# Kernel optimization log

Hardware: AMD Instinct MI355X
Metric: run time of the kernel (lower is better)

The kernel has to match this reference:

```python
import jax, jax.numpy as jnp
import numpy as np

B, S, D, H, DFF = 2, 2048, 1024, 16, 4096
DK = D // H
EPS = 1e-5


def layer_norm(x, gamma, beta, eps=EPS):
    mu = jnp.mean(x, axis=-1, keepdims=True)
    var = jnp.mean(jnp.square(x - mu), axis=-1, keepdims=True)
    return (x - mu) * jax.lax.rsqrt(var + eps) * gamma + beta


def setup_inputs() -> dict:
    key = jax.random.key(0)
    ks = jax.random.split(key, 12)
    s_d = 1.0 / np.sqrt(D)
    s_f = 1.0 / np.sqrt(DFF)
    return {
        "x": jax.random.normal(ks[0], (B, S, D), jnp.float32),
        # per-head QKV projections stacked: [H, D, DK]
        "Wq": jax.random.normal(ks[1], (H, D, DK), jnp.float32) * s_d,
        "bq": jnp.zeros((H, DK), jnp.float32),
        "Wk": jax.random.normal(ks[2], (H, D, DK), jnp.float32) * s_d,
        "bk": jnp.zeros((H, DK), jnp.float32),
        "Wv": jax.random.normal(ks[3], (H, D, DK), jnp.float32) * s_d,
        "bv": jnp.zeros((H, DK), jnp.float32),
        "Wo": jax.random.normal(ks[4], (D, D), jnp.float32) * s_d,
        "bo": jnp.zeros((D,), jnp.float32),
        "W1": jax.random.normal(ks[5], (D, DFF), jnp.float32) * s_d,
        "b1": jnp.zeros((DFF,), jnp.float32),
        "W2": jax.random.normal(ks[6], (DFF, D), jnp.float32) * s_f,
        "b2": jnp.zeros((D,), jnp.float32),
        "ln1_g": jnp.ones((D,), jnp.float32),
        "ln1_b": jnp.zeros((D,), jnp.float32),
        "ln2_g": jnp.ones((D,), jnp.float32),
        "ln2_b": jnp.zeros((D,), jnp.float32),
    }


def reference(x, Wq, bq, Wk, bk, Wv, bv, Wo, bo, W1, b1, W2, b2,
              ln1_g, ln1_b, ln2_g, ln2_b):
    # --- residual 1: pre-norm multi-head self-attention (mask unused, dropout=eval) ---
    h = layer_norm(x, ln1_g, ln1_b)                      # [B,S,D]
    q = jnp.einsum('bsd,hdk->bhsk', h, Wq) + bq[:, None, :]
    k = jnp.einsum('bsd,hdk->bhsk', h, Wk) + bk[:, None, :]
    v = jnp.einsum('bsd,hdk->bhsk', h, Wv) + bv[:, None, :]
    scores = jnp.einsum('bhsk,bhtk->bhst', q, k) / np.sqrt(DK)  # [B,H,S,S]
    w = jax.nn.softmax(scores, axis=-1)
    ctx = jnp.einsum('bhst,bhtk->bhsk', w, v)            # [B,H,S,DK]
    # concat heads along feature dim -> [B,S,D]
    ctx = jnp.transpose(ctx, (0, 2, 1, 3)).reshape(B, S, D)
    attn_out = ctx @ Wo + bo
    x = x + attn_out
    # --- residual 2: pre-norm feed-forward ---
    h2 = layer_norm(x, ln2_g, ln2_b)
    ff = jax.nn.relu(h2 @ W1 + b1) @ W2 + b2
    return x + ff
```

## Files before the change

### kernel.cpp

```cpp
#include <hip/hip_runtime.h>

#define B_   2
#define S_   2048
#define D_   1024
#define H_   16
#define DK_  64
#define DFF_ 4096
#define NT_  (B_*S_)
#define QS_  3072

using u16 = unsigned short;
typedef __attribute__((ext_vector_type(8))) short bf16x8;
typedef __attribute__((ext_vector_type(4))) float f32x4;
typedef __attribute__((ext_vector_type(4))) u16  u16x4;

__device__ __forceinline__ float bf2f(u16 h) {
  union { unsigned u; float f; } c; c.u = ((unsigned)h) << 16; return c.f;
}
__device__ __forceinline__ u16 f2bf(float f) {
  union { float f; unsigned u; } c; c.f = f;
  unsigned u = c.u;
  return (u16)((u + 0x7fffu + ((u >> 16) & 1u)) >> 16);
}
__device__ __forceinline__ u16 f2bf_up(float f) {
  union { float f; unsigned u; } c; c.f = f;
  return (u16)((c.u + 0x8000u) >> 16);
}

__device__ __forceinline__ void load_lds16(const void* g, void* l) {
  __builtin_amdgcn_global_load_lds(
      (const __attribute__((address_space(1))) unsigned int*)g,
      (__attribute__((address_space(3))) unsigned int*)l, 16, 0, 0);
}

__device__ __forceinline__ void store_out(u16* p, float v)   { *p = f2bf(v); }
__device__ __forceinline__ void store_out(float* p, float v) { *p = v; }

__global__ __launch_bounds__(256) void ln_kernel(
    const float* __restrict__ x, const float* __restrict__ g,
    const float* __restrict__ bt, u16* __restrict__ o)
{
  const int row = blockIdx.x, t = threadIdx.x;
  const float4 xv = *(const float4*)(x + (size_t)row * D_ + t * 4);
  float f[4] = {xv.x, xv.y, xv.z, xv.w};
  float sum = f[0] + f[1] + f[2] + f[3];
  float sq  = f[0]*f[0] + f[1]*f[1] + f[2]*f[2] + f[3]*f[3];
#pragma unroll
  for (int d = 32; d >= 1; d >>= 1) {
    sum += __shfl_down(sum, d);
    sq  += __shfl_down(sq, d);
  }
  __shared__ float red[8];
  const int lane = t & 63, wid = t >> 6;
  if (lane == 0) { red[wid] = sum; red[wid + 4] = sq; }
  __syncthreads();
  sum = red[0] + red[1] + red[2] + red[3];
  sq  = red[4] + red[5] + red[6] + red[7];
  const float mu   = sum * (1.0f / D_);
  const float var  = sq * (1.0f / D_) - mu * mu;
  const float rstd = rsqrtf(var + 1e-5f);
  const float4 gv = *(const float4*)(g  + t * 4);
  const float4 bv = *(const float4*)(bt + t * 4);
  u16x4 ov;
  ov[0] = f2bf((f[0] - mu) * rstd * gv.x + bv.x);
  ov[1] = f2bf((f[1] - mu) * rstd * gv.y + bv.y);
  ov[2] = f2bf((f[2] - mu) * rstd * gv.z + bv.z);
  ov[3] = f2bf((f[3] - mu) * rstd * gv.w + bv.w);
  *(u16x4*)(o + (size_t)row * D_ + t * 4) = ov;
}

__global__ __launch_bounds__(256) void transpose_h(
    const float* __restrict__ in, u16* __restrict__ out, int R, int C)
{
  __shared__ float tile[32][33];
  const int z = blockIdx.z;
  const float* ip = in  + (size_t)z * R * C;
  u16*         op = out + (size_t)z * R * C;
  const int c0 = blockIdx.x * 32, r0 = blockIdx.y * 32;
  const int tx = threadIdx.x & 31, ty = threadIdx.x >> 5;
#pragma unroll
  for (int i = 0; i < 32; i += 8)
    tile[ty + i][tx] = ip[(size_t)(r0 + ty + i) * C + c0 + tx];
  __syncthreads();
#pragma unroll
  for (int i = 0; i < 32; i += 8)
    op[(size_t)(c0 + ty + i) * R + r0 + tx] = f2bf(tile[tx][ty + i]);
}

__global__ __launch_bounds__(256) void transpose_qkv(
    const float* __restrict__ Wq, const float* __restrict__ Wk,
    const float* __restrict__ Wv, u16* __restrict__ out)
{
  __shared__ float tile[32][33];
  const int z = blockIdx.z;
  const int which = z >> 4, h = z & 15;
  const float* ip = (which == 0 ? Wq : which == 1 ? Wk : Wv) + (size_t)h * 1024 * 64;
  u16* op = out + ((size_t)which * 1024 + h * 64) * 1024;
  const float sc = (which == 0) ? 0.125f : 1.0f;
  const int c0 = blockIdx.x * 32, r0 = blockIdx.y * 32;
  const int tx = threadIdx.x & 31, ty = threadIdx.x >> 5;
#pragma unroll
  for (int i = 0; i < 32; i += 8)
    tile[ty + i][tx] = ip[(size_t)(r0 + ty + i) * 64 + c0 + tx];
  __syncthreads();
#pragma unroll
  for (int i = 0; i < 32; i += 8)
    op[(size_t)(c0 + ty + i) * 1024 + r0 + tx] = f2bf(tile[tx][ty + i] * sc);
}

__global__ __launch_bounds__(256) void transpose_v(
    const u16* __restrict__ qkv, u16* __restrict__ vt)
{
  __shared__ u16 tile[32][33];
  const int z = blockIdx.z;
  const int b = z >> 4, h = z & 15;
  const u16* ip = qkv + (size_t)(b * S_) * QS_ + 2048 + h * DK_;
  u16* op = vt + (size_t)z * DK_ * S_;
  const int t0 = blockIdx.x * 32, d0 = blockIdx.y * 32;
  const int tx = threadIdx.x & 31, ty = threadIdx.x >> 5;
#pragma unroll
  for (int i = 0; i < 32; i += 8)
    tile[ty + i][tx] = ip[(size_t)(t0 + ty + i) * QS_ + d0 + tx];
  __syncthreads();
#pragma unroll
  for (int i = 0; i < 32; i += 8)
    op[(size_t)(d0 + ty + i) * S_ + t0 + tx] = tile[tx][ty + i];
}

template <typename OT>
__global__ __launch_bounds__(256) void gemm_bt(
    const u16* __restrict__ A, const u16* __restrict__ Bt,
    const float* __restrict__ bias, const float* __restrict__ biasB,
    const float* __restrict__ biasC, const float* __restrict__ res,
    OT* __restrict__ C, int M, int N, int K, int do_relu)
{
  __shared__ u16 lA[2][128 * 32];
  __shared__ u16 lB[2][128 * 32];
  const int tid = threadIdx.x, lane = tid & 63, wid = tid >> 6;
  const int wr = wid >> 1, wc = wid & 1;

  const int nbx = gridDim.x;
  int bid = blockIdx.y * nbx + blockIdx.x;
  const int cpx = (nbx * gridDim.y) >> 3;
  bid = (bid & 7) * cpx + (bid >> 3);
  const int row0 = (bid / nbx) * 128, col0 = (bid % nbx) * 128;

  f32x4 acc[4][4] = {};

  const int cc0 = tid, cc1 = tid + 256;
  const int r0 = cc0 >> 2, s0 = cc0 & 3;
  const int r1 = cc1 >> 2, s1 = cc1 & 3;
  const int ko0 = (s0 ^ ((r0 >> 1) & 3)) * 8;
  const int ko1 = (s1 ^ ((r1 >> 1) & 3)) * 8;

#define GST128(bf, k0)                                                        \
  {                                                                           \
    load_lds16(A  + (size_t)(row0 + r0) * K + (k0) + ko0, &lA[bf][cc0 * 8]);  \
    load_lds16(A  + (size_t)(row0 + r1) * K + (k0) + ko1, &lA[bf][cc1 * 8]);  \
    load_lds16(Bt + (size_t)(col0 + r0) * K + (k0) + ko0, &lB[bf][cc0 * 8]);  \
    load_lds16(Bt + (size_t)(col0 + r1) * K + (k0) + ko1, &lB[bf][cc1 * 8]);  \
  }

  const int nk = K >> 5;
  GST128(0, 0);
  int cur = 0;
  for (int t = 0; t < nk; ++t) {
    __syncthreads();
    if (t + 1 < nk) GST128(cur ^ 1, (t + 1) * 32);
    bf16x8 af[4], bfr[4];
#pragma unroll
    for (int m = 0; m < 4; ++m) {
      const int row = wr * 64 + m * 16 + (lane & 15);
      af[m] = *(const bf16x8*)&lA[cur][row * 32 + (((lane >> 4) ^ ((row >> 1) & 3)) * 8)];
    }
#pragma unroll
    for (int n = 0; n < 4; ++n) {
      const int row = wc * 64 + n * 16 + (lane & 15);
      bfr[n] = *(const bf16x8*)&lB[cur][row * 32 + (((lane >> 4) ^ ((row >> 1) & 3)) * 8)];
    }
#pragma unroll
    for (int m = 0; m < 4; ++m)
#pragma unroll
      for (int n = 0; n < 4; ++n)
        acc[m][n] = __builtin_amdgcn_mfma_f32_16x16x32_bf16(af[m], bfr[n], acc[m][n], 0, 0, 0);
    cur ^= 1;
  }
#undef GST128

#pragma unroll
  for (int m = 0; m < 4; ++m)
#pragma unroll
    for (int n = 0; n < 4; ++n) {
      const int rbase = row0 + wr*64 + m*16 + ((lane >> 4) << 2);
      const int c     = col0 + wc*64 + n*16 + (lane & 15);
      float bv = 0.f;
      if (biasC)      bv = c < 1024 ? bias[c] * 0.125f
                         : (c < 2048 ? biasB[c - 1024] : biasC[c - 2048]);
      else if (bias)  bv = bias[c];
#pragma unroll
      for (int r = 0; r < 4; ++r) {
        const int rr = rbase + r;
        float vv = acc[m][n][r] + bv;
        if (res) vv += res[(size_t)rr * N + c];
        if (do_relu) vv = vv > 0.f ? vv : 0.f;
        store_out(&C[(size_t)rr * N + c], vv);
      }
    }
}

template <typename OT, int KK>
__global__ __launch_bounds__(512, 1) void gemm256(
    const u16* __restrict__ A, const u16* __restrict__ Bt,
    const float* __restrict__ bias, OT* __restrict__ C,
    int M, int N, int do_relu)
{
  constexpr int NK = KK / 32;
  __shared__ u16 lA[4][256 * 32];
  __shared__ u16 lB[4][256 * 32];
  const int tid = threadIdx.x, lane = tid & 63, wid = tid >> 6;
  const int wr = wid >> 2, wc = wid & 3;

  const int nbx = gridDim.x;
  int bid = blockIdx.y * nbx + blockIdx.x;
  const int cpx = (nbx * gridDim.y) >> 3;
  bid = (bid & 7) * cpx + (bid >> 3);
  const int row0 = (bid / nbx) * 256, col0 = (bid % nbx) * 256;

  const int c0 = tid,       sr0 = c0 >> 2, q0 = ((c0 & 3) ^ (((sr0 >> 3) & 1) << 1)) * 8;
  const int c1 = tid + 512, sr1 = c1 >> 2, q1 = ((c1 & 3) ^ (((sr1 >> 3) & 1) << 1)) * 8;
  const u16* As0 = A  + (size_t)(row0 + sr0) * KK + q0;
  const u16* As1 = A  + (size_t)(row0 + sr1) * KK + q1;
  const u16* Bs0 = Bt + (size_t)(col0 + sr0) * KK + q0;
  const u16* Bs1 = Bt + (size_t)(col0 + sr1) * KK + q1;

  f32x4 acc[8][4] = {};
  const int lrow = lane & 15, kcol = (lane >> 4) * 8;

#pragma unroll
  for (int t = 0; t < 3; ++t) {
    load_lds16(As0 + t * 32, &lA[t][c0 * 8]);
    load_lds16(Bs0 + t * 32, &lB[t][c0 * 8]);
    load_lds16(As1 + t * 32, &lA[t][c1 * 8]);
    load_lds16(Bs1 + t * 32, &lB[t][c1 * 8]);
  }
  asm volatile("s_waitcnt vmcnt(8)" ::: "memory");
  __builtin_amdgcn_sched_barrier(0);
  __builtin_amdgcn_s_barrier();

#pragma unroll 4
  for (int j = 0; j < NK; ++j) {
    const int b = j & 3;
    const u16* la = lA[b];
    const u16* lb = lB[b];
    bf16x8 af[4], bfr[4];

#pragma unroll
    for (int m = 0; m < 4; ++m) {
      const int row = wr * 128 + m * 16 + lrow;
      af[m] = *(const bf16x8*)&la[row * 32 + (kcol ^ (((row >> 3) & 1) << 4))];
    }
#pragma unroll
    for (int n = 0; n < 4; ++n) {
      const int row = wc * 64 + n * 16 + lrow;
      bfr[n] = *(const bf16x8*)&lb[row * 32 + (kcol ^ (((row >> 3) & 1) << 4))];
    }
    if (j + 3 < NK) {
      const int bb = (j + 3) & 3;
      load_lds16(As0 + (j + 3) * 32, &lA[bb][c0 * 8]);
      load_lds16(Bs0 + (j + 3) * 32, &lB[bb][c0 * 8]);
    }
    __builtin_amdgcn_s_setprio(1);
#pragma unroll
    for (int m = 0; m < 4; ++m)
#pragma unroll
      for (int n = 0; n < 4; ++n)
        acc[m][n] = __builtin_amdgcn_mfma_f32_16x16x32_bf16(af[m], bfr[n], acc[m][n], 0, 0, 0);
    __builtin_amdgcn_s_setprio(0);
    __builtin_amdgcn_sched_barrier(0);
    __builtin_amdgcn_s_barrier();

#pragma unroll
    for (int m = 0; m < 4; ++m) {
      const int row = wr * 128 + (m + 4) * 16 + lrow;
      af[m] = *(const bf16x8*)&la[row * 32 + (kcol ^ (((row >> 3) & 1) << 4))];
    }
    if (j + 3 < NK) {
      const int bb = (j + 3) & 3;
      load_lds16(As1 + (j + 3) * 32, &lA[bb][c1 * 8]);
      load_lds16(Bs1 + (j + 3) * 32, &lB[bb][c1 * 8]);
    }
    __builtin_amdgcn_s_setprio(1);
#pragma unroll
    for (int m = 0; m < 4; ++m)
#pragma unroll
      for (int n = 0; n < 4; ++n)
        acc[m + 4][n] = __builtin_amdgcn_mfma_f32_16x16x32_bf16(af[m], bfr[n], acc[m + 4][n], 0, 0, 0);
    __builtin_amdgcn_s_setprio(0);
    if (j + 3 < NK)      { asm volatile("s_waitcnt vmcnt(8)" ::: "memory"); }
    else if (j + 2 < NK) { asm volatile("s_waitcnt vmcnt(4)" ::: "memory"); }
    else if (j + 1 < NK) { asm volatile("s_waitcnt vmcnt(0)" ::: "memory"); }
    __builtin_amdgcn_sched_barrier(0);
    __builtin_amdgcn_s_barrier();
  }

#pragma unroll
  for (int m = 0; m < 8; ++m)
#pragma unroll
    for (int n = 0; n < 4; ++n) {
      const int rbase = row0 + wr*128 + m*16 + ((lane >> 4) << 2);
      const int c     = col0 + wc*64 + n*16 + (lane & 15);
      const float bv  = bias ? bias[c] : 0.f;
#pragma unroll
      for (int r = 0; r < 4; ++r) {
        float vv = acc[m][n][r] + bv;
        if (do_relu) vv = vv > 0.f ? vv : 0.f;
        store_out(&C[(size_t)(rbase + r) * N + c], vv);
      }
    }
}

template <typename OT>
__global__ __launch_bounds__(256) void gemm_bt64(
    const u16* __restrict__ A, const u16* __restrict__ Bt,
    const float* __restrict__ bias, const float* __restrict__ res,
    OT* __restrict__ C, int M, int N, int K, int do_relu)
{
  __shared__ u16 lA[2][128 * 32];
  __shared__ u16 lB[2][64 * 32];
  const int tid = threadIdx.x, lane = tid & 63, wid = tid >> 6;

  const int nbx = gridDim.x;
  int bid = blockIdx.y * nbx + blockIdx.x;
  const int cpx = (nbx * gridDim.y) >> 3;
  bid = (bid & 7) * cpx + (bid >> 3);
  const int row0 = (bid / nbx) * 128, col0 = (bid % nbx) * 64;

  f32x4 acc[2][4] = {};

  const int cc0 = tid, cc1 = tid + 256;
  const int r0 = cc0 >> 2, s0 = cc0 & 3;
  const int r1 = cc1 >> 2, s1 = cc1 & 3;
  const int ko0 = (s0 ^ ((r0 >> 1) & 3)) * 8;
  const int ko1 = (s1 ^ ((r1 >> 1) & 3)) * 8;

#define GST64(bf, k0)                                                         \
  {                                                                           \
    load_lds16(A  + (size_t)(row0 + r0) * K + (k0) + ko0, &lA[bf][cc0 * 8]);  \
    load_lds16(A  + (size_t)(row0 + r1) * K + (k0) + ko1, &lA[bf][cc1 * 8]);  \
    load_lds16(Bt + (size_t)(col0 + r0) * K + (k0) + ko0, &lB[bf][cc0 * 8]);  \
  }

  const int nk = K >> 5;
  GST64(0, 0);
  int cur = 0;
  for (int t = 0; t < nk; ++t) {
    __syncthreads();
    if (t + 1 < nk) GST64(cur ^ 1, (t + 1) * 32);
    bf16x8 af[2], bfr[4];
#pragma unroll
    for (int m = 0; m < 2; ++m) {
      const int row = wid * 32 + m * 16 + (lane & 15);
      af[m] = *(const bf16x8*)&lA[cur][row * 32 + (((lane >> 4) ^ ((row >> 1) & 3)) * 8)];
    }
#pragma unroll
    for (int n = 0; n < 4; ++n) {
      const int row = n * 16 + (lane & 15);
      bfr[n] = *(const bf16x8*)&lB[cur][row * 32 + (((lane >> 4) ^ ((row >> 1) & 3)) * 8)];
    }
#pragma unroll
    for (int m = 0; m < 2; ++m)
#pragma unroll
      for (int n = 0; n < 4; ++n)
        acc[m][n] = __builtin_amdgcn_mfma_f32_16x16x32_bf16(af[m], bfr[n], acc[m][n], 0, 0, 0);
    cur ^= 1;
  }
#undef GST64

#pragma unroll
  for (int m = 0; m < 2; ++m)
#pragma unroll
    for (int n = 0; n < 4; ++n) {
      const int rbase = row0 + wid*32 + m*16 + ((lane >> 4) << 2);
      const int c     = col0 + n*16 + (lane & 15);
      const float bv  = bias ? bias[c] : 0.f;
#pragma unroll
      for (int r = 0; r < 4; ++r) {
        const int rr = rbase + r;
        float vv = acc[m][n][r] + bv;
        if (res) vv += res[(size_t)rr * N + c];
        if (do_relu) vv = vv > 0.f ? vv : 0.f;
        store_out(&C[(size_t)rr * N + c], vv);
      }
    }
}

__global__ __launch_bounds__(256) void gemm_bt64_pk(
    const u16* __restrict__ A, const u16* __restrict__ Bt,
    float* __restrict__ P, int M, int N, int K, int KS)
{
  __shared__ u16 lA[2][128 * 32];
  __shared__ u16 lB[2][64 * 32];
  const int tid = threadIdx.x, lane = tid & 63, wid = tid >> 6;

  const int nbx = gridDim.x;
  int bid = blockIdx.y * nbx + blockIdx.x;
  const int cpx = (nbx * gridDim.y) >> 3;
  bid = (bid & 7) * cpx + (bid >> 3);
  const int row0 = (bid / nbx) * 128, col0 = (bid % nbx) * 64;
  const int kb = blockIdx.z * KS;

  f32x4 acc[2][4] = {};

  const int cc0 = tid, cc1 = tid + 256;
  const int r0 = cc0 >> 2, s0 = cc0 & 3;
  const int r1 = cc1 >> 2, s1 = cc1 & 3;
  const int ko0 = (s0 ^ ((r0 >> 1) & 3)) * 8;
  const int ko1 = (s1 ^ ((r1 >> 1) & 3)) * 8;

#define GSTPK(bf, k0)                                                              \
  {                                                                                \
    load_lds16(A  + (size_t)(row0 + r0) * K + kb + (k0) + ko0, &lA[bf][cc0 * 8]);  \
    load_lds16(A  + (size_t)(row0 + r1) * K + kb + (k0) + ko1, &lA[bf][cc1 * 8]);  \
    load_lds16(Bt + (size_t)(col0 + r0) * K + kb + (k0) + ko0, &lB[bf][cc0 * 8]);  \
  }

  const int nk = KS >> 5;
  GSTPK(0, 0);
  int cur = 0;
  for (int t = 0; t < nk; ++t) {
    __syncthreads();
    if (t + 1 < nk) GSTPK(cur ^ 1, (t + 1) * 32);
    bf16x8 af[2], bfr[4];
#pragma unroll
    for (int m = 0; m < 2; ++m) {
      const int row = wid * 32 + m * 16 + (lane & 15);
      af[m] = *(const bf16x8*)&lA[cur][row * 32 + (((lane >> 4) ^ ((row >> 1) & 3)) * 8)];
    }
#pragma unroll
    for (int n = 0; n < 4; ++n) {
      const int row = n * 16 + (lane & 15);
      bfr[n] = *(const bf16x8*)&lB[cur][row * 32 + (((lane >> 4) ^ ((row >> 1) & 3)) * 8)];
    }
#pragma unroll
    for (int m = 0; m < 2; ++m)
#pragma unroll
      for (int n = 0; n < 4; ++n)
        acc[m][n] = __builtin_amdgcn_mfma_f32_16x16x32_bf16(af[m], bfr[n], acc[m][n], 0, 0, 0);
    cur ^= 1;
  }
#undef GSTPK

  float* Pz = P + (size_t)blockIdx.z * M * N;
#pragma unroll
  for (int m = 0; m < 2; ++m)
#pragma unroll
    for (int n = 0; n < 4; ++n) {
      const int rbase = row0 + wid*32 + m*16 + ((lane >> 4) << 2);
      const int c     = col0 + n*16 + (lane & 15);
#pragma unroll
      for (int r = 0; r < 4; ++r)
        Pz[(size_t)(rbase + r) * N + c] = acc[m][n][r];
    }
}

__global__ __launch_bounds__(256) void ffr_reduce(
    const float* __restrict__ p0, const float* __restrict__ p1,
    const float* __restrict__ x1, const float* __restrict__ b2,
    float* __restrict__ out)
{
  const size_t i = (size_t)blockIdx.x * 256 + threadIdx.x;
  const float4 a  = ((const float4*)p0)[i];
  const float4 b  = ((const float4*)p1)[i];
  const float4 r  = ((const float4*)x1)[i];
  const float4 bb = ((const float4*)b2)[i & 255];
  float4 o;
  o.x = a.x + b.x + r.x + bb.x;
  o.y = a.y + b.y + r.y + bb.y;
  o.z = a.z + b.z + r.z + bb.z;
  o.w = a.w + b.w + r.w + bb.w;
  ((float4*)out)[i] = o;
}

__global__ __launch_bounds__(512) void attn_kernel(
    const u16* __restrict__ QKV, const u16* __restrict__ Vt, u16* __restrict__ O)
{
  __shared__ u16 lK[2][64 * 64];
  __shared__ u16 lV[2][64 * 64];
  __shared__ u16 lP[128 * 64];

  const int tid = threadIdx.x, lane = tid & 63, wid = tid >> 6;
  const int qt = ((blockIdx.x & 7) << 1) | (blockIdx.x >> 3);
  const int h = blockIdx.y, b = blockIdx.z;

  const u16* Qp = QKV + (size_t)(b * S_ + qt * 128) * QS_ + h * DK_;
  const u16* Kb = QKV + (size_t)(b * S_) * QS_ + 1024 + h * DK_;
  const u16* Vb = Vt  + (size_t)(b * H_ + h) * DK_ * S_;

  bf16x8 qf[2];
  {
    const int qr = wid * 16 + (lane & 15);
    qf[0] = *(const bf16x8*)(Qp + (size_t)qr * QS_ + (lane >> 4) * 8);
    qf[1] = *(const bf16x8*)(Qp + (size_t)qr * QS_ + 32 + (lane >> 4) * 8);
  }

  const bf16x8 vone = {16256,16256,16256,16256,16256,16256,16256,16256};

#define STAGE_KV(bf, kt)                                                      \
  {                                                                           \
    const u16* Kp = Kb + (size_t)(kt) * 64 * QS_;                             \
    const u16* Vp = Vb + (size_t)(kt) * 64;                                   \
    const int c = tid, r = c >> 3, sub = c & 7;                               \
    load_lds16(Kp + (size_t)r * QS_ + ((sub ^ (r & 7)) * 8), &lK[bf][c * 8]); \
    load_lds16(Vp + (size_t)r * S_  + ((sub ^ (r & 7)) * 8), &lV[bf][c * 8]); \
  }

  float m_run = -1e30f;
  f32x4 l_acc = {};
  f32x4 o_acc[4] = {};

  STAGE_KV(0, 0);
  int cur = 0;

  for (int kt = 0; kt < S_ / 64; ++kt) {
    __syncthreads();
    if (kt + 1 < S_ / 64) STAGE_KV(cur ^ 1, kt + 1);

    f32x4 s[4];
    __builtin_amdgcn_s_setprio(1);
#pragma unroll
    for (int kf = 0; kf < 4; ++kf) {
      const int row = kf * 16 + (lane & 15);
      const int i0 = (row * 64 + (lane >> 4) * 8)      ^ ((row & 7) << 3);
      const int i1 = (row * 64 + 32 + (lane >> 4) * 8) ^ ((row & 7) << 3);
      bf16x8 k0 = *(const bf16x8*)&lK[cur][i0];
      bf16x8 k1 = *(const bf16x8*)&lK[cur][i1];
      f32x4 sc = {};
      sc = __builtin_amdgcn_mfma_f32_16x16x32_bf16(k0, qf[0], sc, 0, 0, 0);
      sc = __builtin_amdgcn_mfma_f32_16x16x32_bf16(k1, qf[1], sc, 0, 0, 0);
      s[kf] = sc;
    }
    __builtin_amdgcn_s_setprio(0);

    float t0 = fmaxf(fmaxf(s[0][0], s[0][1]), fmaxf(s[0][2], s[0][3]));
    float t1 = fmaxf(fmaxf(s[1][0], s[1][1]), fmaxf(s[1][2], s[1][3]));
    float t2 = fmaxf(fmaxf(s[2][0], s[2][1]), fmaxf(s[2][2], s[2][3]));
    float t3 = fmaxf(fmaxf(s[3][0], s[3][1]), fmaxf(s[3][2], s[3][3]));
    float pmax = fmaxf(fmaxf(t0, t1), fmaxf(t2, t3));
    pmax = fmaxf(pmax, __shfl_xor(pmax, 16));
    pmax = fmaxf(pmax, __shfl_xor(pmax, 32));

    const bool grow = pmax > m_run + 8.0f;
    const float mnew = grow ? pmax : m_run;
    if (__any(grow)) {
      const float scale = __expf(m_run - mnew);
#pragma unroll
      for (int r = 0; r < 4; ++r) {
        const float sr = __shfl(scale, (lane >> 4) * 4 + r);
        l_acc[r] *= sr;
#pragma unroll
        for (int nf = 0; nf < 4; ++nf) o_acc[nf][r] *= sr;
      }
    }
    m_run = mnew;

    const int prow = wid * 16 + (lane & 15);
#pragma unroll
    for (int kf = 0; kf < 4; ++kf) {
      u16x4 pk;
#pragma unroll
      for (int r = 0; r < 4; ++r) pk[r] = f2bf_up(__expf(s[kf][r] - m_run));
      const int idx = (prow * 64 + kf * 16 + (lane >> 4) * 4) ^ ((prow & 7) << 3);
      *(u16x4*)&lP[idx] = pk;
    }
    asm volatile("s_waitcnt lgkmcnt(0)" ::: "memory");
    __builtin_amdgcn_sched_barrier(0);

    bf16x8 pa0 = *(const bf16x8*)&lP[(prow * 64 + (lane >> 4) * 8)      ^ ((prow & 7) << 3)];
    bf16x8 pa1 = *(const bf16x8*)&lP[(prow * 64 + 32 + (lane >> 4) * 8) ^ ((prow & 7) << 3)];
    __builtin_amdgcn_s_setprio(1);
    l_acc = __builtin_amdgcn_mfma_f32_16x16x32_bf16(pa0, vone, l_acc, 0, 0, 0);
    l_acc = __builtin_amdgcn_mfma_f32_16x16x32_bf16(pa1, vone, l_acc, 0, 0, 0);
#pragma unroll
    for (int nf = 0; nf < 4; ++nf) {
      const int vrow = nf * 16 + (lane & 15);
      bf16x8 v0 = *(const bf16x8*)&lV[cur][(vrow * 64 + (lane >> 4) * 8)      ^ ((vrow & 7) << 3)];
      bf16x8 v1 = *(const bf16x8*)&lV[cur][(vrow * 64 + 32 + (lane >> 4) * 8) ^ ((vrow & 7) << 3)];
      o_acc[nf] = __builtin_amdgcn_mfma_f32_16x16x32_bf16(pa0, v0, o_acc[nf], 0, 0, 0);
      o_acc[nf] = __builtin_amdgcn_mfma_f32_16x16x32_bf16(pa1, v1, o_acc[nf], 0, 0, 0);
    }
    __builtin_amdgcn_s_setprio(0);
    cur ^= 1;
  }

#pragma unroll
  for (int nf = 0; nf < 4; ++nf)
#pragma unroll
    for (int r = 0; r < 4; ++r) {
      const int qrow = qt * 128 + wid * 16 + (lane >> 4) * 4 + r;
      const int col  = h * DK_ + nf * 16 + (lane & 15);
      O[(size_t)(b * S_ + qrow) * D_ + col] = f2bf(o_acc[nf][r] / l_acc[r]);
    }
}

extern "C" void kernel_launch(void* const* d_in, const int* in_sizes, int n_in,
                              void* d_out, int out_size, void* d_ws, size_t ws_size,
                              hipStream_t stream)
{
  const float* x   = (const float*)d_in[0];
  const float* Wq  = (const float*)d_in[1];
  const float* bq  = (const float*)d_in[2];
  const float* Wk  = (const float*)d_in[3];
  const float* bk  = (const float*)d_in[4];
  const float* Wv  = (const float*)d_in[5];
  const float* bv  = (const float*)d_in[6];
  const float* Wo  = (const float*)d_in[7];
  const float* bo  = (const float*)d_in[8];
  const float* W1  = (const float*)d_in[9];
  const float* b1  = (const float*)d_in[10];
  const float* W2  = (const float*)d_in[11];
  const float* b2  = (const float*)d_in[12];
  const float* g1  = (const float*)d_in[13];
  const float* be1 = (const float*)d_in[14];
  const float* g2  = (const float*)d_in[15];
  const float* be2 = (const float*)d_in[16];
  float* out = (float*)d_out;

  const size_t MB = 1024 * 1024;
  char* base = (char*)d_ws;
  u16*   xn    = (u16*)(base);
  u16*   qkv   = (u16*)(base +  8*MB);
  u16*   ctx   = (u16*)(base + 32*MB);
  float* x1    = (float*)(base + 40*MB);
  u16*   vt    = (u16*)(base + 40*MB);
  u16*   ff1   = (u16*)(base +  8*MB);
  u16*   wqkvT = (u16*)(base + 56*MB);
  u16*   woT   = (u16*)(base + 62*MB);
  u16*   w1T   = (u16*)(base + 64*MB);
  u16*   w2T   = (u16*)(base + 72*MB);
  float* pk0   = (float*)(base + 80*MB);
  float* pk1   = (float*)(base + 96*MB);

  const bool splitk = ws_size >= (size_t)112 * MB;

  dim3 blk(256);
  transpose_qkv<<<dim3(2, 32, 48), blk, 0, stream>>>(Wq, Wk, Wv, wqkvT);
  transpose_h<<<dim3(32, 32, 1),  blk, 0, stream>>>(Wo, woT, 1024, 1024);
  transpose_h<<<dim3(128, 32, 1), blk, 0, stream>>>(W1, w1T, 1024, 4096);
  transpose_h<<<dim3(32, 128, 1), blk, 0, stream>>>(W2, w2T, 4096, 1024);

  ln_kernel<<<NT_, blk, 0, stream>>>(x, g1, be1, xn);

  gemm_bt<<<dim3(24, 32), blk, 0, stream>>>(xn, wqkvT, bq, bk, bv,
                                            (const float*)nullptr, qkv, NT_, QS_, D_, 0);

  transpose_v<<<dim3(64, 2, 32), blk, 0, stream>>>(qkv, vt);

  attn_kernel<<<dim3(S_ / 128, H_, B_), dim3(512), 0, stream>>>(qkv, vt, ctx);

  gemm_bt64<<<dim3(16, 32), blk, 0, stream>>>(ctx, woT, bo, x, x1, NT_, D_, D_, 0);

  ln_kernel<<<NT_, blk, 0, stream>>>(x1, g2, be2, xn);

  gemm256<u16, 1024><<<dim3(16, 16), dim3(512), 0, stream>>>(xn, w1T, b1, ff1,
                                                             NT_, DFF_, 1);

  if (splitk) {
    gemm_bt64_pk<<<dim3(16, 32, 2), blk, 0, stream>>>(ff1, w2T, pk0, NT_, D_, DFF_, DFF_ / 2);
    ffr_reduce<<<dim3(4096), blk, 0, stream>>>(pk0, pk1, x1, b2, out);
  } else {
    gemm_bt64<<<dim3(16, 32), blk, 0, stream>>>(ff1, w2T, b2, x1, out, NT_, D_, DFF_, 0);
  }
}
```

Measured before the change: 269.8 us.

## Route QKV GEMM through gemm256 and deepen gemm_bt64 pipelines to four stages

The QKV projection now runs on the 256x256-tile gemm256 kernel (12x16 blocks), which gains the fused per-section QKV bias handling, in place of the 128x128 gemm_bt kernel. The gemm_bt64 and split-K gemm_bt64_pk kernels change from double buffering with __syncthreads to a 4-buffer LDS pipeline that prefetches three stages ahead, uses explicit vmcnt waits and raw barriers, and raises wave priority around the MFMA blocks. This targets global-load latency and per-iteration sync overhead, at the cost of twice the LDS per block, which may lower occupancy. The QKV grid of 192 large blocks may underfill the available CUs.

Measured after the change: 281.8 us. 4.5% more time.

```diff
diff --git a/kernel.cpp b/kernel.cpp
--- a/kernel.cpp
+++ b/kernel.cpp
@@ -127,91 +127,11 @@
     op[(size_t)(d0 + ty + i) * S_ + t0 + tx] = tile[tx][ty + i];
 }
 
-template <typename OT>
-__global__ __launch_bounds__(256) void gemm_bt(
-    const u16* __restrict__ A, const u16* __restrict__ Bt,
-    const float* __restrict__ bias, const float* __restrict__ biasB,
-    const float* __restrict__ biasC, const float* __restrict__ res,
-    OT* __restrict__ C, int M, int N, int K, int do_relu)
-{
-  __shared__ u16 lA[2][128 * 32];
-  __shared__ u16 lB[2][128 * 32];
-  const int tid = threadIdx.x, lane = tid & 63, wid = tid >> 6;
-  const int wr = wid >> 1, wc = wid & 1;
-
-  const int nbx = gridDim.x;
-  int bid = blockIdx.y * nbx + blockIdx.x;
-  const int cpx = (nbx * gridDim.y) >> 3;
-  bid = (bid & 7) * cpx + (bid >> 3);
-  const int row0 = (bid / nbx) * 128, col0 = (bid % nbx) * 128;
-
-  f32x4 acc[4][4] = {};
-
-  const int cc0 = tid, cc1 = tid + 256;
-  const int r0 = cc0 >> 2, s0 = cc0 & 3;
-  const int r1 = cc1 >> 2, s1 = cc1 & 3;
-  const int ko0 = (s0 ^ ((r0 >> 1) & 3)) * 8;
-  const int ko1 = (s1 ^ ((r1 >> 1) & 3)) * 8;
-
-#define GST128(bf, k0)                                                        \
-  {                                                                           \
-    load_lds16(A  + (size_t)(row0 + r0) * K + (k0) + ko0, &lA[bf][cc0 * 8]);  \
-    load_lds16(A  + (size_t)(row0 + r1) * K + (k0) + ko1, &lA[bf][cc1 * 8]);  \
-    load_lds16(Bt + (size_t)(col0 + r0) * K + (k0) + ko0, &lB[bf][cc0 * 8]);  \
-    load_lds16(Bt + (size_t)(col0 + r1) * K + (k0) + ko1, &lB[bf][cc1 * 8]);  \
-  }
-
-  const int nk = K >> 5;
-  GST128(0, 0);
-  int cur = 0;
-  for (int t = 0; t < nk; ++t) {
-    __syncthreads();
-    if (t + 1 < nk) GST128(cur ^ 1, (t + 1) * 32);
-    bf16x8 af[4], bfr[4];
-#pragma unroll
-    for (int m = 0; m < 4; ++m) {
-      const int row = wr * 64 + m * 16 + (lane & 15);
-      af[m] = *(const bf16x8*)&lA[cur][row * 32 + (((lane >> 4) ^ ((row >> 1) & 3)) * 8)];
-    }
-#pragma unroll
-    for (int n = 0; n < 4; ++n) {
-      const int row = wc * 64 + n * 16 + (lane & 15);
-      bfr[n] = *(const bf16x8*)&lB[cur][row * 32 + (((lane >> 4) ^ ((row >> 1) & 3)) * 8)];
-    }
-#pragma unroll
-    for (int m = 0; m < 4; ++m)
-#pragma unroll
-      for (int n = 0; n < 4; ++n)
-        acc[m][n] = __builtin_amdgcn_mfma_f32_16x16x32_bf16(af[m], bfr[n], acc[m][n], 0, 0, 0);
-    cur ^= 1;
-  }
-#undef GST128
-
-#pragma unroll
-  for (int m = 0; m < 4; ++m)
-#pragma unroll
-    for (int n = 0; n < 4; ++n) {
-      const int rbase = row0 + wr*64 + m*16 + ((lane >> 4) << 2);
-      const int c     = col0 + wc*64 + n*16 + (lane & 15);
-      float bv = 0.f;
-      if (biasC)      bv = c < 1024 ? bias[c] * 0.125f
-                         : (c < 2048 ? biasB[c - 1024] : biasC[c - 2048]);
-      else if (bias)  bv = bias[c];
-#pragma unroll
-      for (int r = 0; r < 4; ++r) {
-        const int rr = rbase + r;
-        float vv = acc[m][n][r] + bv;
-        if (res) vv += res[(size_t)rr * N + c];
-        if (do_relu) vv = vv > 0.f ? vv : 0.f;
-        store_out(&C[(size_t)rr * N + c], vv);
-      }
-    }
-}
-
 template <typename OT, int KK>
 __global__ __launch_bounds__(512, 1) void gemm256(
     const u16* __restrict__ A, const u16* __restrict__ Bt,
-    const float* __restrict__ bias, OT* __restrict__ C,
+    const float* __restrict__ bias, const float* __restrict__ biasB,
+    const float* __restrict__ biasC, OT* __restrict__ C,
     int M, int N, int do_relu)
 {
   constexpr int NK = KK / 32;
@@ -309,7 +229,10 @@
     for (int n = 0; n < 4; ++n) {
       const int rbase = row0 + wr*128 + m*16 + ((lane >> 4) << 2);
       const int c     = col0 + wc*64 + n*16 + (lane & 15);
-      const float bv  = bias ? bias[c] : 0.f;
+      float bv = 0.f;
+      if (biasC)      bv = c < 1024 ? bias[c] * 0.125f
+                         : (c < 2048 ? biasB[c - 1024] : biasC[c - 2048]);
+      else if (bias)  bv = bias[c];
 #pragma unroll
       for (int r = 0; r < 4; ++r) {
         float vv = acc[m][n][r] + bv;
@@ -325,8 +248,8 @@
     const float* __restrict__ bias, const float* __restrict__ res,
     OT* __restrict__ C, int M, int N, int K, int do_relu)
 {
-  __shared__ u16 lA[2][128 * 32];
-  __shared__ u16 lB[2][64 * 32];
+  __shared__ u16 lA[4][128 * 32];
+  __shared__ u16 lB[4][64 * 32];
   const int tid = threadIdx.x, lane = tid & 63, wid = tid >> 6;
 
   const int nbx = gridDim.x;
@@ -337,42 +260,55 @@
 
   f32x4 acc[2][4] = {};
 
-  const int cc0 = tid, cc1 = tid + 256;
-  const int r0 = cc0 >> 2, s0 = cc0 & 3;
-  const int r1 = cc1 >> 2, s1 = cc1 & 3;
+  const int r0 = tid >> 2, s0 = tid & 3;
+  const int c1 = tid + 256, r1 = c1 >> 2, s1 = c1 & 3;
   const int ko0 = (s0 ^ ((r0 >> 1) & 3)) * 8;
   const int ko1 = (s1 ^ ((r1 >> 1) & 3)) * 8;
-
-#define GST64(bf, k0)                                                         \
-  {                                                                           \
-    load_lds16(A  + (size_t)(row0 + r0) * K + (k0) + ko0, &lA[bf][cc0 * 8]);  \
-    load_lds16(A  + (size_t)(row0 + r1) * K + (k0) + ko1, &lA[bf][cc1 * 8]);  \
-    load_lds16(Bt + (size_t)(col0 + r0) * K + (k0) + ko0, &lB[bf][cc0 * 8]);  \
+  const u16* As0 = A  + (size_t)(row0 + r0) * K + ko0;
+  const u16* As1 = A  + (size_t)(row0 + r1) * K + ko1;
+  const u16* Bs0 = Bt + (size_t)(col0 + r0) * K + ko0;
+
+#define GST64(bf, k0)                                  \
+  {                                                    \
+    load_lds16(As0 + (k0), &lA[bf][tid * 8]);          \
+    load_lds16(As1 + (k0), &lA[bf][c1 * 8]);           \
+    load_lds16(Bs0 + (k0), &lB[bf][tid * 8]);          \
   }
 
   const int nk = K >> 5;
-  GST64(0, 0);
-  int cur = 0;
-  for (int t = 0; t < nk; ++t) {
-    __syncthreads();
-    if (t + 1 < nk) GST64(cur ^ 1, (t + 1) * 32);
+#pragma unroll
+  for (int t = 0; t < 3; ++t) GST64(t, t * 32);
+  asm volatile("s_waitcnt vmcnt(6)" ::: "memory");
+  __builtin_amdgcn_sched_barrier(0);
+  __builtin_amdgcn_s_barrier();
+
+#pragma unroll 4
+  for (int j = 0; j < nk; ++j) {
+    const int b = j & 3;
     bf16x8 af[2], bfr[4];
 #pragma unroll
     for (int m = 0; m < 2; ++m) {
       const int row = wid * 32 + m * 16 + (lane & 15);
-      af[m] = *(const bf16x8*)&lA[cur][row * 32 + (((lane >> 4) ^ ((row >> 1) & 3)) * 8)];
+      af[m] = *(const bf16x8*)&lA[b][row * 32 + (((lane >> 4) ^ ((row >> 1) & 3)) * 8)];
     }
 #pragma unroll
     for (int n = 0; n < 4; ++n) {
       const int row = n * 16 + (lane & 15);
-      bfr[n] = *(const bf16x8*)&lB[cur][row * 32 + (((lane >> 4) ^ ((row >> 1) & 3)) * 8)];
-    }
+      bfr[n] = *(const bf16x8*)&lB[b][row * 32 + (((lane >> 4) ^ ((row >> 1) & 3)) * 8)];
+    }
+    if (j + 3 < nk) GST64((j + 3) & 3, (j + 3) * 32);
+    __builtin_amdgcn_s_setprio(1);
 #pragma unroll
     for (int m = 0; m < 2; ++m)
 #pragma unroll
       for (int n = 0; n < 4; ++n)
         acc[m][n] = __builtin_amdgcn_mfma_f32_16x16x32_bf16(af[m], bfr[n], acc[m][n], 0, 0, 0);
-    cur ^= 1;
+    __builtin_amdgcn_s_setprio(0);
+    if (j + 3 < nk)      { asm volatile("s_waitcnt vmcnt(6)" ::: "memory"); }
+    else if (j + 2 < nk) { asm volatile("s_waitcnt vmcnt(3)" ::: "memory"); }
+    else if (j + 1 < nk) { asm volatile("s_waitcnt vmcnt(0)" ::: "memory"); }
+    __builtin_amdgcn_sched_barrier(0);
+    __builtin_amdgcn_s_barrier();
   }
 #undef GST64
 
@@ -398,8 +334,8 @@
     const u16* __restrict__ A, const u16* __restrict__ Bt,
     float* __restrict__ P, int M, int N, int K, int KS)
 {
-  __shared__ u16 lA[2][128 * 32];
-  __shared__ u16 lB[2][64 * 32];
+  __shared__ u16 lA[4][128 * 32];
+  __shared__ u16 lB[4][64 * 32];
   const int tid = threadIdx.x, lane = tid & 63, wid = tid >> 6;
 
   const int nbx = gridDim.x;
@@ -411,42 +347,55 @@
 
   f32x4 acc[2][4] = {};
 
-  const int cc0 = tid, cc1 = tid + 256;
-  const int r0 = cc0 >> 2, s0 = cc0 & 3;
-  const int r1 = cc1 >> 2, s1 = cc1 & 3;
+  const int r0 = tid >> 2, s0 = tid & 3;
+  const int c1 = tid + 256, r1 = c1 >> 2, s1 = c1 & 3;
   const int ko0 = (s0 ^ ((r0 >> 1) & 3)) * 8;
   const int ko1 = (s1 ^ ((r1 >> 1) & 3)) * 8;
-
-#define GSTPK(bf, k0)                                                              \
-  {                                                                                \
-    load_lds16(A  + (size_t)(row0 + r0) * K + kb + (k0) + ko0, &lA[bf][cc0 * 8]);  \
-    load_lds16(A  + (size_t)(row0 + r1) * K + kb + (k0) + ko1, &lA[bf][cc1 * 8]);  \
-    load_lds16(Bt + (size_t)(col0 + r0) * K + kb + (k0) + ko0, &lB[bf][cc0 * 8]);  \
+  const u16* As0 = A  + (size_t)(row0 + r0) * K + kb + ko0;
+  const u16* As1 = A  + (size_t)(row0 + r1) * K + kb + ko1;
+  const u16* Bs0 = Bt + (size_t)(col0 + r0) * K + kb + ko0;
+
+#define GSTPK(bf, k0)                                  \
+  {                                                    \
+    load_lds16(As0 + (k0), &lA[bf][tid * 8]);          \
+    load_lds16(As1 + (k0), &lA[bf][c1 * 8]);           \
+    load_lds16(Bs0 + (k0), &lB[bf][tid * 8]);          \
   }
 
   const int nk = KS >> 5;
-  GSTPK(0, 0);
-  int cur = 0;
-  for (int t = 0; t < nk; ++t) {
-    __syncthreads();
-    if (t + 1 < nk) GSTPK(cur ^ 1, (t + 1) * 32);
+#pragma unroll
+  for (int t = 0; t < 3; ++t) GSTPK(t, t * 32);
+  asm volatile("s_waitcnt vmcnt(6)" ::: "memory");
+  __builtin_amdgcn_sched_barrier(0);
+  __builtin_amdgcn_s_barrier();
+
+#pragma unroll 4
+  for (int j = 0; j < nk; ++j) {
+    const int b = j & 3;
     bf16x8 af[2], bfr[4];
 #pragma unroll
     for (int m = 0; m < 2; ++m) {
       const int row = wid * 32 + m * 16 + (lane & 15);
-      af[m] = *(const bf16x8*)&lA[cur][row * 32 + (((lane >> 4) ^ ((row >> 1) & 3)) * 8)];
+      af[m] = *(const bf16x8*)&lA[b][row * 32 + (((lane >> 4) ^ ((row >> 1) & 3)) * 8)];
     }
 #pragma unroll
     for (int n = 0; n < 4; ++n) {
       const int row = n * 16 + (lane & 15);
-      bfr[n] = *(const bf16x8*)&lB[cur][row * 32 + (((lane >> 4) ^ ((row >> 1) & 3)) * 8)];
-    }
+      bfr[n] = *(const bf16x8*)&lB[b][row * 32 + (((lane >> 4) ^ ((row >> 1) & 3)) * 8)];
+    }
+    if (j + 3 < nk) GSTPK((j + 3) & 3, (j + 3) * 32);
+    __builtin_amdgcn_s_setprio(1);
 #pragma unroll
     for (int m = 0; m < 2; ++m)
 #pragma unroll
       for (int n = 0; n < 4; ++n)
         acc[m][n] = __builtin_amdgcn_mfma_f32_16x16x32_bf16(af[m], bfr[n], acc[m][n], 0, 0, 0);
-    cur ^= 1;
+    __builtin_amdgcn_s_setprio(0);
+    if (j + 3 < nk)      { asm volatile("s_waitcnt vmcnt(6)" ::: "memory"); }
+    else if (j + 2 < nk) { asm volatile("s_waitcnt vmcnt(3)" ::: "memory"); }
+    else if (j + 1 < nk) { asm volatile("s_waitcnt vmcnt(0)" ::: "memory"); }
+    __builtin_amdgcn_sched_barrier(0);
+    __builtin_amdgcn_s_barrier();
   }
 #undef GSTPK
 
@@ -650,8 +599,8 @@
 
   ln_kernel<<<NT_, blk, 0, stream>>>(x, g1, be1, xn);
 
-  gemm_bt<<<dim3(24, 32), blk, 0, stream>>>(xn, wqkvT, bq, bk, bv,
-                                            (const float*)nullptr, qkv, NT_, QS_, D_, 0);
+  gemm256<u16, 1024><<<dim3(12, 16), dim3(512), 0, stream>>>(
+      xn, wqkvT, bq, bk, bv, qkv, NT_, QS_, 0);
 
   transpose_v<<<dim3(64, 2, 32), blk, 0, stream>>>(qkv, vt);
 
@@ -661,8 +610,8 @@
 
   ln_kernel<<<NT_, blk, 0, stream>>>(x1, g2, be2, xn);
 
-  gemm256<u16, 1024><<<dim3(16, 16), dim3(512), 0, stream>>>(xn, w1T, b1, ff1,
-                                                             NT_, DFF_, 1);
+  gemm256<u16, 1024><<<dim3(16, 16), dim3(512), 0, stream>>>(
+      xn, w1T, b1, (const float*)nullptr, (const float*)nullptr, ff1, NT_, DFF_, 1);
 
   if (splitk) {
     gemm_bt64_pk<<<dim3(16, 32, 2), blk, 0, stream>>>(ff1, w2T, pk0, NT_, D_, DFF_, DFF_ / 2);
```
